# Optimization experiments

Measured on AMD Instinct MI355X. Metric: run time of the kernel, lower is better.

The kernel has to match this reference:

```python
import jax, jax.numpy as jnp
import numpy as np


def setup_inputs() -> dict:
    key = jax.random.key(0)
    k1, k2, k3 = jax.random.split(key, 3)
    B, H, L, D = 4, 16, 1024, 64
    q = jax.random.normal(k1, (B, H, L, D), dtype=jnp.float32)
    k = jax.random.normal(k2, (B, H, L, D), dtype=jnp.float32)
    attn_mask = jax.random.randint(k3, (B, H, L, L), 0, 2).astype(bool)
    return {"q": q, "k": k, "attn_mask": attn_mask}


def reference(q, k, attn_mask):
    # q, k: [B, H, L, D]. The original builds a [B,H,L,D,L] tensor
    # c[b,h,i,m,j] = exp(-(q[b,h,i,m]-k[b,h,j,m])^2), then for each dim m
    # keeps only the entries where rank of q[i,m] (along seq) equals rank of
    # k[j,m], scatters them into an LxL grid and averages over m.
    # Equivalent fused form: sort q and k per dimension, pair equal ranks,
    # and scatter-add exp(-(q_sorted - k_sorted)^2)/D into p[b,h,i,j].
    B, H, L, D = q.shape
    q_idx = jnp.argsort(q, axis=2)                       # [B,H,L,D] int
    k_idx = jnp.argsort(k, axis=2)
    q_sorted = jnp.take_along_axis(q, q_idx, axis=2)     # [B,H,L,D]
    k_sorted = jnp.take_along_axis(k, k_idx, axis=2)
    diff = q_sorted - k_sorted
    vals = jnp.exp(-(diff * diff))                       # [B,H,L,D]
    # linear index into the flattened [L,L] grid, plus batch*head offset
    lin = q_idx * L + k_idx                              # [B,H,L,D]
    bh_off = (jnp.arange(B * H) * (L * L)).reshape(B, H, 1, 1)
    flat_idx = (lin + bh_off).ravel()
    p = jnp.zeros(B * H * L * L, dtype=q.dtype).at[flat_idx].add(vals.ravel())
    p = (p / D).reshape(B, H, L, L)
    return jnp.where(attn_mask, jnp.zeros((), dtype=p.dtype), p)
```

## Files before the change

kernel.cpp:

```cpp
#include <hip/hip_runtime.h>
#include <stdint.h>
#include <string.h>


#define LL 1024
#define DD 64
#define NBH 64
#define MAT_WORDS ((size_t)NBH * DD * LL)
#define WS_BYTES (3 * MAT_WORDS * 4)

typedef float    vf4   __attribute__((ext_vector_type(4)));
typedef uint32_t vu4   __attribute__((ext_vector_type(4)));
typedef int32_t  vi4   __attribute__((ext_vector_type(4)));

__device__ __forceinline__ uint32_t f2ord(float x) {
    uint32_t u = __float_as_uint(x);
    return (u & 0x80000000u) ? ~u : (u | 0x80000000u);
}
__device__ __forceinline__ float ord2f(uint32_t o) {
    uint32_t u = (o & 0x80000000u) ? (o & 0x7fffffffu) : ~o;
    return __uint_as_float(u);
}

template <int CTRL>
__device__ __forceinline__ uint64_t dpp64(uint64_t v) {
    const uint32_t lo = (uint32_t)__builtin_amdgcn_update_dpp(
        0, (int)(uint32_t)v, CTRL, 0xF, 0xF, true);
    const uint32_t hi = (uint32_t)__builtin_amdgcn_update_dpp(
        0, (int)(uint32_t)(v >> 32), CTRL, 0xF, 0xF, true);
    return ((uint64_t)hi << 32) | lo;
}
template <int PATT>
__device__ __forceinline__ uint64_t swz64(uint64_t v) {
    const uint32_t lo = (uint32_t)__builtin_amdgcn_ds_swizzle(
        (int)(uint32_t)v, PATT);
    const uint32_t hi = (uint32_t)__builtin_amdgcn_ds_swizzle(
        (int)(uint32_t)(v >> 32), PATT);
    return ((uint64_t)hi << 32) | lo;
}
__device__ __forceinline__ uint64_t bper64(uint64_t v, int addr) {
    const uint32_t lo = (uint32_t)__builtin_amdgcn_ds_bpermute(
        addr, (int)(uint32_t)v);
    const uint32_t hi = (uint32_t)__builtin_amdgcn_ds_bpermute(
        addr, (int)(uint32_t)(v >> 32));
    return ((uint64_t)hi << 32) | lo;
}
__device__ __forceinline__ uint64_t fx1 (uint64_t v){ return dpp64<0xB1>(v); }
__device__ __forceinline__ uint64_t fx2 (uint64_t v){ return dpp64<0x4E>(v); }
__device__ __forceinline__ uint64_t fx3 (uint64_t v){ return dpp64<0x1B>(v); }
__device__ __forceinline__ uint64_t fx4 (uint64_t v){ return dpp64<0x1B>(dpp64<0x141>(v)); }
__device__ __forceinline__ uint64_t fx7 (uint64_t v){ return dpp64<0x141>(v); }
__device__ __forceinline__ uint64_t fx8 (uint64_t v){ return dpp64<0x141>(dpp64<0x140>(v)); }
__device__ __forceinline__ uint64_t fx15(uint64_t v){ return dpp64<0x140>(v); }
__device__ __forceinline__ uint64_t fx16(uint64_t v){ return swz64<0x401F>(v); }
__device__ __forceinline__ uint64_t fx31(uint64_t v){ return swz64<0x7C1F>(v); }

__device__ __forceinline__ void wave_sort1024(uint64_t x[16], const int lane,
                                              const int addr63)
{
    auto cexA = [](uint64_t& a, uint64_t& b) {
        const uint64_t lo = a < b ? a : b;
        const uint64_t hi = a < b ? b : a;
        a = lo; b = hi;
    };
    auto sel = [](uint64_t xv, uint64_t y, bool km) {
        return ((xv < y) == km) ? xv : y;
    };

#define TAIL4() do { _Pragma("unroll") \
    for (int j = 8; j >= 1; j >>= 1) { _Pragma("unroll") \
        for (int s = 0; s < 16; ++s) \
            if (!(s & j)) cexA(x[s], x[s | j]); } } while (0)

#define MIRROR(F, KM) do { _Pragma("unroll") \
    for (int i = 0; i < 8; ++i) { \
        const uint64_t ya = F(x[15 - i]); \
        const uint64_t yb = F(x[i]); \
        x[i]      = sel(x[i],      ya, (KM)); \
        x[15 - i] = sel(x[15 - i], yb, (KM)); } } while (0)

#define XORST(F, KM) do { _Pragma("unroll") \
    for (int s = 0; s < 16; ++s) { \
        const uint64_t y = F(x[s]); \
        x[s] = sel(x[s], y, (KM)); } } while (0)

    #pragma unroll
    for (int s = 0; s < 16; s += 2) cexA(x[s], x[s + 1]);
    #pragma unroll
    for (int b = 0; b < 16; b += 4) {
        cexA(x[b], x[b + 3]); cexA(x[b + 1], x[b + 2]);
    }
    #pragma unroll
    for (int s = 0; s < 16; s += 2) cexA(x[s], x[s + 1]);
    #pragma unroll
    for (int b = 0; b < 16; b += 8) {
        cexA(x[b], x[b + 7]); cexA(x[b + 1], x[b + 6]);
        cexA(x[b + 2], x[b + 5]); cexA(x[b + 3], x[b + 4]);
    }
    #pragma unroll
    for (int j = 2; j >= 1; j >>= 1) {
        #pragma unroll
        for (int s = 0; s < 16; ++s)
            if (!(s & j)) cexA(x[s], x[s | j]);
    }
    #pragma unroll
    for (int i = 0; i < 8; ++i) cexA(x[i], x[15 - i]);
    #pragma unroll
    for (int j = 4; j >= 1; j >>= 1) {
        #pragma unroll
        for (int s = 0; s < 16; ++s)
            if (!(s & j)) cexA(x[s], x[s | j]);
    }

    { const bool km = (lane & 1) == 0;
      MIRROR(fx1, km); TAIL4(); }
    { const bool kmM = (lane & 2) == 0;
      MIRROR(fx3, kmM);
      const bool k1 = (lane & 1) == 0; XORST(fx1, k1); TAIL4(); }
    { const bool kmM = (lane & 4) == 0;
      MIRROR(fx7, kmM);
      const bool k2 = (lane & 2) == 0; XORST(fx2, k2);
      const bool k1 = (lane & 1) == 0; XORST(fx1, k1); TAIL4(); }
    { const bool kmM = (lane & 8) == 0;
      MIRROR(fx15, kmM);
      const bool k4 = (lane & 4) == 0; XORST(fx4, k4);
      const bool k2 = (lane & 2) == 0; XORST(fx2, k2);
      const bool k1 = (lane & 1) == 0; XORST(fx1, k1); TAIL4(); }
    { const bool kmM = (lane & 16) == 0;
      MIRROR(fx31, kmM);
      const bool k8 = (lane & 8) == 0; XORST(fx8, k8);
      const bool k4 = (lane & 4) == 0; XORST(fx4, k4);
      const bool k2 = (lane & 2) == 0; XORST(fx2, k2);
      const bool k1 = (lane & 1) == 0; XORST(fx1, k1); TAIL4(); }
    { const bool kmM = (lane & 32) == 0;
      #pragma unroll
      for (int i = 0; i < 8; ++i) {
          const uint64_t ya = bper64(x[15 - i], addr63);
          const uint64_t yb = bper64(x[i], addr63);
          x[i]      = sel(x[i],      ya, kmM);
          x[15 - i] = sel(x[15 - i], yb, kmM);
      }
      const bool k16 = (lane & 16) == 0; XORST(fx16, k16);
      const bool k8  = (lane & 8)  == 0; XORST(fx8,  k8);
      const bool k4  = (lane & 4)  == 0; XORST(fx4,  k4);
      const bool k2  = (lane & 2)  == 0; XORST(fx2,  k2);
      const bool k1  = (lane & 1)  == 0; XORST(fx1,  k1); TAIL4(); }

#undef TAIL4
#undef MIRROR
#undef XORST
}

__global__ __launch_bounds__(256) void swd3_transpose(
    const float* __restrict__ q, const float* __restrict__ k,
    uint32_t* __restrict__ qt, uint32_t* __restrict__ kt)
{
    __shared__ uint32_t tq[64][65];
    __shared__ uint32_t tk[64][65];

    const int b  = blockIdx.x;
    const int bh = (b & 7) * 8 + ((b >> 3) & 7);
    const int e0 = (b >> 6) * 64;
    const int t  = threadIdx.x;

    const size_t base = (size_t)bh * (LL * DD);
    #pragma unroll
    for (int i = 0; i < 4; ++i) {
        const int idx = i * 256 + t;
        const int r   = idx >> 4;
        const int c   = (idx & 15) * 4;
        const vf4 vq = *(const vf4*)(q + base + (size_t)(e0 + r) * DD + c);
        const vf4 vk = *(const vf4*)(k + base + (size_t)(e0 + r) * DD + c);
        tq[r][c + 0] = f2ord(vq.x); tq[r][c + 1] = f2ord(vq.y);
        tq[r][c + 2] = f2ord(vq.z); tq[r][c + 3] = f2ord(vq.w);
        tk[r][c + 0] = f2ord(vk.x); tk[r][c + 1] = f2ord(vk.y);
        tk[r][c + 2] = f2ord(vk.z); tk[r][c + 3] = f2ord(vk.w);
    }
    __syncthreads();
    #pragma unroll
    for (int i = 0; i < 4; ++i) {
        const int idx = i * 256 + t;
        const int d   = idx >> 4;
        const int c   = (idx & 15) * 4;
        vu4 v;
        v.x = tq[c + 0][d]; v.y = tq[c + 1][d];
        v.z = tq[c + 2][d]; v.w = tq[c + 3][d];
        *(vu4*)(qt + base + (size_t)d * LL + e0 + c) = v;
        v.x = tk[c + 0][d]; v.y = tk[c + 1][d];
        v.z = tk[c + 2][d]; v.w = tk[c + 3][d];
        *(vu4*)(kt + base + (size_t)d * LL + e0 + c) = v;
    }
}

__global__ __launch_bounds__(256, 3) void swd3_phase1(
    const uint32_t* __restrict__ qt, const uint32_t* __restrict__ kt,
    uint32_t* __restrict__ pairs)
{
    __shared__ alignas(16) uint32_t pr[4][LL];

    const int raw  = blockIdx.x;
    const int slot = raw >> 3;
    const int bh   = (raw & 7) * 8 + (slot >> 4);
    const int dg   = slot & 15;
    const int t    = threadIdx.x;
    const int w    = t >> 6;
    const int lane = t & 63;
    const int d    = dg * 4 + w;
    const int addr63 = (lane ^ 63) << 2;

    const uint32_t* colq = qt + (size_t)bh * (DD * LL) + (size_t)d * LL;
    const uint32_t* colk = kt + (size_t)bh * (DD * LL) + (size_t)d * LL;

    uint64_t xq[16], xk[16];
    #pragma unroll
    for (int r = 0; r < 4; ++r) {
        const vu4 vq = *(const vu4*)(colq + 256 * r + 4 * lane);
        const vu4 vk = *(const vu4*)(colk + 256 * r + 4 * lane);
        const uint32_t eb = 256u * r + 4u * lane;
        xq[4 * r + 0] = ((uint64_t)vq.x << 32) | (eb + 0);
        xq[4 * r + 1] = ((uint64_t)vq.y << 32) | (eb + 1);
        xq[4 * r + 2] = ((uint64_t)vq.z << 32) | (eb + 2);
        xq[4 * r + 3] = ((uint64_t)vq.w << 32) | (eb + 3);
        xk[4 * r + 0] = ((uint64_t)vk.x << 32) | (eb + 0);
        xk[4 * r + 1] = ((uint64_t)vk.y << 32) | (eb + 1);
        xk[4 * r + 2] = ((uint64_t)vk.z << 32) | (eb + 2);
        xk[4 * r + 3] = ((uint64_t)vk.w << 32) | (eb + 3);
    }
    wave_sort1024(xq, lane, addr63);
    wave_sort1024(xk, lane, addr63);

    uint32_t* prw = pr[w];
    #pragma unroll
    for (int s = 0; s < 16; ++s) {
        const uint32_t iq = (uint32_t)xq[s] & 1023u;
        const uint32_t ik = (uint32_t)xk[s] & 1023u;
        const float df = ord2f((uint32_t)(xq[s] >> 32))
                       - ord2f((uint32_t)(xk[s] >> 32));
        const float val = __expf(-df * df) * (1.0f / 64.0f);
        prw[iq] = (__float_as_uint(val) & 0xFFFFFC00u) | ik;
    }
    __asm__ volatile("s_waitcnt lgkmcnt(0)" ::: "memory");
    vu4* pp4 = (vu4*)(pairs + ((size_t)bh * DD + d) * LL);
    const vu4* src = (const vu4*)prw;
    #pragma unroll
    for (int r = 0; r < 4; ++r)
        pp4[r * 64 + lane] = src[r * 64 + lane];
}

__global__ __launch_bounds__(256) void swd3_phase2(
    const uint32_t* __restrict__ pairs, const void* __restrict__ maskp,
    float* __restrict__ out)
{
    __shared__ alignas(16) float acc[8 * LL];
    __shared__ uint32_t sdet[4];

    const int b  = blockIdx.x;
    const int bh = (b & 7) * 8 + ((b >> 3) & 7);
    const int st = b >> 6;
    const int i0 = st * 8;
    const int t  = threadIdx.x;

    {
        const uint32_t w = ((const uint32_t*)maskp)[t];
        const uint64_t bal = __ballot(w > 1u);
        if ((t & 63) == 0) sdet[t >> 6] = (bal != 0ull) ? 1u : 0u;
    }

    vf4* acc4 = (vf4*)acc;
    #pragma unroll
    for (int v = 0; v < 8; ++v) {
        vf4 z; z.x = 0.f; z.y = 0.f; z.z = 0.f; z.w = 0.f;
        acc4[v * 256 + t] = z;
    }
    __syncthreads();

    const bool mask_byte =
        ((sdet[0] | sdet[1] | sdet[2] | sdet[3]) != 0u);
    const size_t cellbase = ((size_t)bh << 20) + ((size_t)i0 << 10);

    uint32_t mb[8];
    vi4      mi[8];
    if (mask_byte) {
        const uint32_t* mp = (const uint32_t*)maskp + (cellbase >> 2);
        #pragma unroll
        for (int v = 0; v < 8; ++v)
            mb[v] = __builtin_nontemporal_load(mp + v * 256 + t);
    } else {
        const vi4* mp = (const vi4*)((const int32_t*)maskp + cellbase);
        #pragma unroll
        for (int v = 0; v < 8; ++v)
            mi[v] = __builtin_nontemporal_load(mp + v * 256 + t);
    }

    {
        const uint32_t* pb = pairs + (size_t)bh * (DD * LL);
        const int dd = t >> 2;
        const uint2 pv = ((const uint2*)(pb + dd * LL + i0))[t & 3];
        const int ii0 = 2 * (t & 3), ii1 = ii0 + 1;
        atomicAdd(&acc[ii0 * LL + (int)(pv.x & 1023u)],
                  __uint_as_float(pv.x & 0xFFFFFC00u));
        atomicAdd(&acc[ii1 * LL + (int)(pv.y & 1023u)],
                  __uint_as_float(pv.y & 0xFFFFFC00u));
    }
    __syncthreads();

    vf4* ob = (vf4*)(out + cellbase);
    #pragma unroll
    for (int v = 0; v < 8; ++v) {
        const int p = v * 256 + t;
        const vf4 a = acc4[p];
        int mx, my, mz, mw2;
        if (mask_byte) {
            const uint32_t m = mb[v];
            mx = (int)(m & 0xFFu); my = (int)((m >> 8) & 0xFFu);
            mz = (int)((m >> 16) & 0xFFu); mw2 = (int)(m >> 24);
        } else {
            mx = mi[v].x; my = mi[v].y; mz = mi[v].z; mw2 = mi[v].w;
        }
        vf4 r;
        r.x = mx  ? 0.f : a.x;
        r.y = my  ? 0.f : a.y;
        r.z = mz  ? 0.f : a.z;
        r.w = mw2 ? 0.f : a.w;
        __builtin_nontemporal_store(r, ob + p);
    }
}

extern "C" void kernel_launch(void* const* d_in, const int* in_sizes, int n_in,
                              void* d_out, int out_size, void* d_ws, size_t ws_size,
                              hipStream_t stream) {
    const float* q = (const float*)d_in[0];
    const float* k = (const float*)d_in[1];
    const void* mask = d_in[2];
    uint32_t* pairs = (uint32_t*)d_ws;
    uint32_t* qt = pairs + MAT_WORDS;
    uint32_t* kt = qt + MAT_WORDS;

    const bool ws_ok = (ws_size >= WS_BYTES);
    hipError_t e0 = hipSuccess, e1 = hipSuccess, e2 = hipSuccess;
    (void)hipGetLastError();

    if (ws_ok) {
        swd3_transpose<<<NBH * 16, 256, 0, stream>>>(q, k, qt, kt);
        e0 = hipGetLastError();
        swd3_phase1<<<NBH * DD / 4, 256, 0, stream>>>(qt, kt, pairs);
        e1 = hipGetLastError();
        swd3_phase2<<<NBH * 128, 256, 0, stream>>>(pairs, mask, (float*)d_out);
        e2 = hipGetLastError();
    }

    if (!ws_ok || e0 != hipSuccess || e1 != hipSuccess || e2 != hipSuccess) {
        static float h_stamp[8];
        h_stamp[0] = !ws_ok ? (9000.0f + (float)(ws_size >> 20))
                            : (1000.0f + (float)(int)e0);
        h_stamp[1] = 2000.0f + (float)(int)e1;
        h_stamp[2] = 3000.0f + (float)(int)e2;
        h_stamp[3] = h_stamp[0];
        hipMemcpyAsync(d_out, h_stamp, sizeof(h_stamp),
                       hipMemcpyHostToDevice, stream);
    }
}
```

Baseline: 508.0 us.

## Restructure phase2 into per-wave row processing without block barriers

Phase2 now has each 64-lane wave own a single 1024-float LDS row buffer and process four output rows one after another. Each row is zeroed, scatter-accumulated, masked and stored using only LDS waitcnts instead of block-wide __syncthreads. The block now covers 16 rows, so the grid is halved, LDS use falls from 32KB to 16KB, and launch bounds request 8 blocks per CU for higher occupancy. The trade-off is less memory-level parallelism per wave, since mask loads are issued per row in a serial loop instead of all up front.

```diff
diff --git a/kernel.cpp b/kernel.cpp
--- a/kernel.cpp
+++ b/kernel.cpp
@@ -247,82 +247,78 @@
         pp4[r * 64 + lane] = src[r * 64 + lane];
 }
 
-__global__ __launch_bounds__(256) void swd3_phase2(
+__global__ __launch_bounds__(256, 8) void swd3_phase2(
     const uint32_t* __restrict__ pairs, const void* __restrict__ maskp,
     float* __restrict__ out)
 {
-    __shared__ alignas(16) float acc[8 * LL];
-    __shared__ uint32_t sdet[4];
-
-    const int b  = blockIdx.x;
-    const int bh = (b & 7) * 8 + ((b >> 3) & 7);
-    const int st = b >> 6;
-    const int i0 = st * 8;
-    const int t  = threadIdx.x;
-
-    {
-        const uint32_t w = ((const uint32_t*)maskp)[t];
-        const uint64_t bal = __ballot(w > 1u);
-        if ((t & 63) == 0) sdet[t >> 6] = (bal != 0ull) ? 1u : 0u;
-    }
-
-    vf4* acc4 = (vf4*)acc;
-    #pragma unroll
-    for (int v = 0; v < 8; ++v) {
-        vf4 z; z.x = 0.f; z.y = 0.f; z.z = 0.f; z.w = 0.f;
-        acc4[v * 256 + t] = z;
-    }
-    __syncthreads();
-
-    const bool mask_byte =
-        ((sdet[0] | sdet[1] | sdet[2] | sdet[3]) != 0u);
-    const size_t cellbase = ((size_t)bh << 20) + ((size_t)i0 << 10);
-
-    uint32_t mb[8];
-    vi4      mi[8];
-    if (mask_byte) {
-        const uint32_t* mp = (const uint32_t*)maskp + (cellbase >> 2);
+    __shared__ alignas(16) float rowbuf[4][LL];
+
+    const int b    = blockIdx.x;
+    const int bh   = (b & 7) * 8 + ((b >> 3) & 7);
+    const int g    = b >> 6;
+    const int t    = threadIdx.x;
+    const int w    = t >> 6;
+    const int lane = t & 63;
+    const int i0   = g * 16 + w * 4;
+
+    const uint32_t dw = ((const uint32_t*)maskp)[lane];
+    const bool mask_byte = (__ballot(dw > 1u) != 0ull);
+
+    const uint32_t* pb = pairs + (size_t)bh * (DD * LL);
+    const vu4 rec = *(const vu4*)(pb + (size_t)lane * LL + i0);
+
+    float* lrow = rowbuf[w];
+    vf4*   l4   = (vf4*)lrow;
+
+    #pragma unroll
+    for (int r = 0; r < 4; ++r) {
+        const int i = i0 + r;
+        const size_t cellrow = ((size_t)bh << 20) + ((size_t)i << 10);
+
+        uint32_t mb[4]; vi4 mi[4];
+        if (mask_byte) {
+            const uint32_t* mp = (const uint32_t*)maskp + (cellrow >> 2);
+            #pragma unroll
+            for (int it = 0; it < 4; ++it)
+                mb[it] = __builtin_nontemporal_load(mp + it * 64 + lane);
+        } else {
+            const vi4* mp = (const vi4*)((const int32_t*)maskp + cellrow);
+            #pragma unroll
+            for (int it = 0; it < 4; ++it)
+                mi[it] = __builtin_nontemporal_load(mp + it * 64 + lane);
+        }
+
         #pragma unroll
-        for (int v = 0; v < 8; ++v)
-            mb[v] = __builtin_nontemporal_load(mp + v * 256 + t);
-    } else {
-        const vi4* mp = (const vi4*)((const int32_t*)maskp + cellbase);
+        for (int it = 0; it < 4; ++it) {
+            vf4 z; z.x = 0.f; z.y = 0.f; z.z = 0.f; z.w = 0.f;
+            l4[it * 64 + lane] = z;
+        }
+        __asm__ volatile("s_waitcnt lgkmcnt(0)" ::: "memory");
+
+        const uint32_t pv = rec[r];
+        atomicAdd(&lrow[pv & 1023u], __uint_as_float(pv & 0xFFFFFC00u));
+        __asm__ volatile("s_waitcnt lgkmcnt(0)" ::: "memory");
+
+        vf4* ob = (vf4*)(out + cellrow);
         #pragma unroll
-        for (int v = 0; v < 8; ++v)
-            mi[v] = __builtin_nontemporal_load(mp + v * 256 + t);
-    }
-
-    {
-        const uint32_t* pb = pairs + (size_t)bh * (DD * LL);
-        const int dd = t >> 2;
-        const uint2 pv = ((const uint2*)(pb + dd * LL + i0))[t & 3];
-        const int ii0 = 2 * (t & 3), ii1 = ii0 + 1;
-        atomicAdd(&acc[ii0 * LL + (int)(pv.x & 1023u)],
-                  __uint_as_float(pv.x & 0xFFFFFC00u));
-        atomicAdd(&acc[ii1 * LL + (int)(pv.y & 1023u)],
-                  __uint_as_float(pv.y & 0xFFFFFC00u));
-    }
-    __syncthreads();
-
-    vf4* ob = (vf4*)(out + cellbase);
-    #pragma unroll
-    for (int v = 0; v < 8; ++v) {
-        const int p = v * 256 + t;
-        const vf4 a = acc4[p];
-        int mx, my, mz, mw2;
-        if (mask_byte) {
-            const uint32_t m = mb[v];
-            mx = (int)(m & 0xFFu); my = (int)((m >> 8) & 0xFFu);
-            mz = (int)((m >> 16) & 0xFFu); mw2 = (int)(m >> 24);
-        } else {
-            mx = mi[v].x; my = mi[v].y; mz = mi[v].z; mw2 = mi[v].w;
+        for (int it = 0; it < 4; ++it) {
+            const vf4 a = l4[it * 64 + lane];
+            int mx, my, mz, mw2;
+            if (mask_byte) {
+                const uint32_t m = mb[it];
+                mx = (int)(m & 0xFFu); my = (int)((m >> 8) & 0xFFu);
+                mz = (int)((m >> 16) & 0xFFu); mw2 = (int)(m >> 24);
+            } else {
+                mx = mi[it].x; my = mi[it].y; mz = mi[it].z; mw2 = mi[it].w;
+            }
+            vf4 rr;
+            rr.x = mx  ? 0.f : a.x;
+            rr.y = my  ? 0.f : a.y;
+            rr.z = mz  ? 0.f : a.z;
+            rr.w = mw2 ? 0.f : a.w;
+            __builtin_nontemporal_store(rr, ob + it * 64 + lane);
         }
-        vf4 r;
-        r.x = mx  ? 0.f : a.x;
-        r.y = my  ? 0.f : a.y;
-        r.z = mz  ? 0.f : a.z;
-        r.w = mw2 ? 0.f : a.w;
-        __builtin_nontemporal_store(r, ob + p);
+        __asm__ volatile("s_waitcnt lgkmcnt(0)" ::: "memory");
     }
 }
 
@@ -345,7 +341,7 @@
         e0 = hipGetLastError();
         swd3_phase1<<<NBH * DD / 4, 256, 0, stream>>>(qt, kt, pairs);
         e1 = hipGetLastError();
-        swd3_phase2<<<NBH * 128, 256, 0, stream>>>(pairs, mask, (float*)d_out);
+        swd3_phase2<<<NBH * 64, 256, 0, stream>>>(pairs, mask, (float*)d_out);
         e2 = hipGetLastError();
     }
 
```

Result: slower. 526.7 us (+3.7%).
